# Kernel tuning notes

Hardware: AMD Instinct MI355X
Metric: run time of the kernel (lower is better)

## Reference

```python
import jax, jax.numpy as jnp
import numpy as np

B, H, W, CIN, CI = 2, 64, 64, 128, 128  # in_channels == inter_channels (required by final gating)
N = H * W
TEMP = 1.0
EPS = 1e-3  # tfa InstanceNormalization default epsilon


def _conv1x1(x, w, b):
    # x: (B,H,W,Cin), w: (Cin,Cout)
    return jnp.einsum('bhwc,cd->bhwd', x, w) + b


def _conv3x3_reflect(x, w, b):
    x = jnp.pad(x, ((0, 0), (1, 1), (1, 1), (0, 0)), mode='reflect')
    y = jax.lax.conv_general_dilated(x, w, (1, 1), 'VALID',
                                     dimension_numbers=('NHWC', 'HWIO', 'NHWC'))
    return y + b


def _instance_norm(x, gamma, beta):
    m = x.mean(axis=(1, 2), keepdims=True)
    v = x.var(axis=(1, 2), keepdims=True)
    return (x - m) * jax.lax.rsqrt(v + EPS) * gamma + beta


def setup_inputs() -> dict:
    key = jax.random.key(0)
    ks = jax.random.split(key, 16)
    p = lambda i, shape: 0.02 * jax.random.normal(ks[i], shape, jnp.float32)
    x = jax.random.normal(ks[0], (B, H, W, CIN), jnp.float32)
    mask = (jax.random.uniform(ks[1], (B, H, W, 1)) > 0.5).astype(jnp.float32)  # binary hole mask
    return dict(
        x=x, mask=mask,
        wg=p(2, (CIN, CI)), bg=jnp.zeros((CI,), jnp.float32),
        wt=p(3, (CIN, CI)), bt=jnp.zeros((CI,), jnp.float32),
        wp=p(4, (CIN, CI)), bp=jnp.zeros((CI,), jnp.float32),
        ww=p(5, (CI, CIN)), bw=jnp.zeros((CIN,), jnp.float32),
        res_w1=p(6, (3, 3, 3, CIN, CIN)), res_b1=jnp.zeros((3, CIN), jnp.float32),
        res_g1=jnp.ones((3, CIN), jnp.float32), res_be1=jnp.zeros((3, CIN), jnp.float32),
        res_w2=p(7, (3, 3, 3, CIN, CIN)), res_b2=jnp.zeros((3, CIN), jnp.float32),
        res_g2=jnp.ones((3, CIN), jnp.float32), res_be2=jnp.zeros((3, CIN), jnp.float32),
    )


def reference(x, mask, wg, bg, wt, bt, wp, bp, ww, bw,
              res_w1, res_b1, res_g1, res_be1,
              res_w2, res_b2, res_g2, res_be2):
    # projections, flatten spatial -> tokens
    g_x = _conv1x1(x, wg, bg).reshape(B, N, CI)      # (B,N,Ci)
    theta = _conv1x1(x, wt, bt).reshape(B, N, CI)    # (B,N,Ci)
    phi = _conv1x1(x, wp, bp).reshape(B, N, CI)      # (B,N,Ci)

    # f_div_C = softmax(theta . phi^T / T) over keys  -> (B,N,N), memory-dominant
    f_div_C = jax.nn.softmax(jnp.einsum('bnc,bmc->bnm', theta, phi) / TEMP, axis=2)

    # mask processing (bilinear resize to x's spatial size; identity here)
    inverted = 1.0 - mask
    m = jax.image.resize(mask, (B, H, W, 1), 'bilinear')
    m = jnp.where(m > 0.0, jnp.zeros_like(m), m)  # zero out any positively-masked pixel
    m = 1.0 - m                                   # 1 where strictly unmasked
    inverted = jax.image.resize(inverted, (B, H, W, 1), 'bilinear')
    m = m * inverted                              # (B,H,W,1)

    # gate attention columns by mask (broadcast over query rows == tf.repeat)
    f_div_C = m.reshape(B, 1, N) * f_div_C

    y = jnp.einsum('bnm,bmc->bnc', f_div_C, g_x).reshape(B, H, W, CI)
    w_y = _conv1x1(y, ww, bw)                     # (B,H,W,Cin)

    # 3 ResNet blocks: reflect-pad conv3x3 -> IN -> ReLU -> reflect-pad conv3x3 -> IN, + residual
    for i in range(3):
        h = jax.nn.relu(_instance_norm(_conv3x3_reflect(w_y, res_w1[i], res_b1[i]),
                                       res_g1[i], res_be1[i]))
        h = _instance_norm(_conv3x3_reflect(h, res_w2[i], res_b2[i]),
                           res_g2[i], res_be2[i])
        w_y = w_y + h

    # mode == 'combine': mask-gated blend of input and attention output
    z = m * x + (1.0 - m) * w_y
    return z
```

## Files before the change

### kernel.cpp

```cpp
#include <hip/hip_runtime.h>
#include <math.h>

constexpr int NB = 2;
constexpr int IMG = 64;
constexpr int CH = 128;
constexpr int NT = IMG * IMG;
constexpr int ATT_KSPLIT = 8;
constexpr int KPS = NT / ATT_KSPLIT;

typedef __bf16 bf16x8 __attribute__((ext_vector_type(8)));
typedef float f32x4 __attribute__((ext_vector_type(4)));

__device__ __forceinline__ unsigned f2bf(float x) {
  unsigned u = __float_as_uint(x);
  return (u + 0x7fffu + ((u >> 16) & 1u)) >> 16;
}
__device__ __forceinline__ float bf2f(unsigned h) {
  return __uint_as_float(h << 16);
}
__device__ __forceinline__ float maskval(float mk) {
  float mm = mk > 0.f ? 0.f : mk;
  return (1.f - mm) * (1.f - mk);
}

__global__ __launch_bounds__(256) void k_prepw(
    const float* __restrict__ rw1, const float* __restrict__ rw2,
    const float* __restrict__ wt_, const float* __restrict__ wp_,
    const float* __restrict__ wg_, const float* __restrict__ ww_,
    unsigned short* __restrict__ wfrag) {
  __shared__ float Ws[128][132];
  const int t = threadIdx.x, bx = blockIdx.x;
  const float* src;
  if (bx < 54) {
    int i2 = bx / 9, tap = bx - i2 * 9;
    int blk = i2 >> 1;
    src = ((i2 & 1) ? rw2 : rw1) + ((size_t)blk * 9 + tap) * 16384;
  } else {
    src = bx == 54 ? wt_ : bx == 55 ? wp_ : bx == 56 ? wg_ : ww_;
  }
#pragma unroll
  for (int k = 0; k < 16; ++k) {
    int i4 = t + 256 * k;
    int row = i4 >> 5, c4 = (i4 & 31) << 2;
    *(float4*)&Ws[row][c4] = *(const float4*)(src + (size_t)row * 128 + c4);
  }
  __syncthreads();
  unsigned short* dst = wfrag + (size_t)bx * 16384;
#pragma unroll
  for (int i = 0; i < 8; ++i) {
    int idx = t + 256 * i;
    int lane = idx & 63, k = (idx >> 6) & 3, cotile = idx >> 8;
    int lg = lane >> 4, lc = lane & 15;
    int co = cotile * 16 + lc, ci0 = k * 32 + lg * 8;
    unsigned u0 = f2bf(Ws[ci0 + 0][co]) | (f2bf(Ws[ci0 + 1][co]) << 16);
    unsigned u1 = f2bf(Ws[ci0 + 2][co]) | (f2bf(Ws[ci0 + 3][co]) << 16);
    unsigned u2 = f2bf(Ws[ci0 + 4][co]) | (f2bf(Ws[ci0 + 5][co]) << 16);
    unsigned u3 = f2bf(Ws[ci0 + 6][co]) | (f2bf(Ws[ci0 + 7][co]) << 16);
    *(uint4*)(dst + (size_t)idx * 8) = make_uint4(u0, u1, u2, u3);
  }
}

__global__ __launch_bounds__(256) void k_proj3(
    const float* __restrict__ x, const float* __restrict__ mask,
    const unsigned short* __restrict__ wf, const float* __restrict__ bt_,
    const float* __restrict__ bp_, const float* __restrict__ bg_,
    unsigned short* __restrict__ thb, unsigned short* __restrict__ phb,
    unsigned short* __restrict__ vtb) {
  __shared__ __align__(16) unsigned short Al[64 * 136];
  __shared__ __align__(16) unsigned short Tl[64 * 136];
  const int t = threadIdx.x, r0 = blockIdx.x * 64, b = r0 >> 12;

#pragma unroll
  for (int k = 0; k < 4; ++k) {
    int it = t + 256 * k;
    int row = it >> 4, g = it & 15;
    const float* s = x + (size_t)(r0 + row) * 128 + g * 8;
    float4 v0 = *(const float4*)s, v1 = *(const float4*)(s + 4);
    uint4 pk;
    pk.x = f2bf(v0.x) | (f2bf(v0.y) << 16);
    pk.y = f2bf(v0.z) | (f2bf(v0.w) << 16);
    pk.z = f2bf(v1.x) | (f2bf(v1.y) << 16);
    pk.w = f2bf(v1.z) | (f2bf(v1.w) << 16);
    *(uint4*)&Al[row * 136 + g * 8] = pk;
  }
  __syncthreads();

  const int w = t >> 6, lane = t & 63, lg = lane >> 4, lc = lane & 15;
  const int mw = w & 1, nw = w >> 1;
#pragma unroll
  for (int mat = 0; mat < 3; ++mat) {
    f32x4 acc[2][4];
#pragma unroll
    for (int m = 0; m < 2; ++m)
#pragma unroll
      for (int n = 0; n < 4; ++n)
#pragma unroll
        for (int r = 0; r < 4; ++r) acc[m][n][r] = 0.f;
    const unsigned short* wb =
        wf + (size_t)(54 + mat) * 16384 + (size_t)(nw * 4) * 2048 + lane * 8;
#pragma unroll
    for (int k = 0; k < 4; ++k) {
      bf16x8 a0 = *(const bf16x8*)&Al[(mw * 32 + lc) * 136 + k * 32 + lg * 8];
      bf16x8 a1 = *(const bf16x8*)&Al[(mw * 32 + 16 + lc) * 136 + k * 32 + lg * 8];
#pragma unroll
      for (int n = 0; n < 4; ++n) {
        bf16x8 bfr = *(const bf16x8*)(wb + n * 2048 + k * 512);
        acc[0][n] = __builtin_amdgcn_mfma_f32_16x16x32_bf16(a0, bfr, acc[0][n], 0, 0, 0);
        acc[1][n] = __builtin_amdgcn_mfma_f32_16x16x32_bf16(a1, bfr, acc[1][n], 0, 0, 0);
      }
    }
    const float* bs = mat == 0 ? bt_ : mat == 1 ? bp_ : bg_;
    float bbv[4];
#pragma unroll
    for (int n = 0; n < 4; ++n) bbv[n] = bs[nw * 64 + n * 16 + lc];

    if (mat < 2) {
      unsigned short* ob = mat == 0 ? thb : phb;
#pragma unroll
      for (int n = 0; n < 4; ++n) {
        int col = nw * 64 + n * 16 + lc;
#pragma unroll
        for (int m = 0; m < 2; ++m)
#pragma unroll
          for (int r = 0; r < 4; ++r) {
            int row = r0 + mw * 32 + m * 16 + lg * 4 + r;
            ob[(size_t)row * 128 + col] = (unsigned short)f2bf(acc[m][n][r] + bbv[n]);
          }
      }
    } else {
#pragma unroll
      for (int m = 0; m < 2; ++m)
#pragma unroll
        for (int r = 0; r < 4; ++r) {
          int rl = mw * 32 + m * 16 + lg * 4 + r;
          float mvv = maskval(mask[r0 + rl]);
#pragma unroll
          for (int n = 0; n < 4; ++n) {
            int col = nw * 64 + n * 16 + lc;
            Tl[rl * 136 + col] = (unsigned short)f2bf((acc[m][n][r] + bbv[n]) * mvv);
          }
        }
      __syncthreads();
      const int c = t >> 1, h = t & 1;
      unsigned buf[16];
#pragma unroll
      for (int j = 0; j < 16; ++j)
        buf[j] = (unsigned)Tl[(h * 32 + 2 * j) * 136 + c] |
                 ((unsigned)Tl[(h * 32 + 2 * j + 1) * 136 + c] << 16);
      const int key0 = r0 & (NT - 1);
      unsigned short* dst = vtb + ((size_t)b * CH + c) * NT + key0 + h * 32;
      uint4* d4 = (uint4*)dst;
#pragma unroll
      for (int q = 0; q < 4; ++q)
        d4[q] = make_uint4(buf[4 * q], buf[4 * q + 1], buf[4 * q + 2], buf[4 * q + 3]);
    }
  }
}

__global__ __launch_bounds__(256, 2) void k_attn(
    const unsigned short* __restrict__ theta, const unsigned short* __restrict__ phi,
    const unsigned short* __restrict__ vt, unsigned short* __restrict__ partO,
    float* __restrict__ partL) {
  __shared__ __align__(16) unsigned short Klds[64][136];
  __shared__ __align__(16) unsigned short Vtlds[128][72];
  __shared__ __align__(16) unsigned short Plds[4][32][72];

  const int t = threadIdx.x;
  const int bx = blockIdx.x;
  const int ks = bx & 7;
  const int qt = (bx >> 3) & 31;
  const int b = bx >> 8;
  const int w = t >> 6;
  const int lane = t & 63;
  const int lg = lane >> 4;
  const int lc = lane & 15;
  const int q0 = qt * 128 + w * 32;

  const unsigned short* thB = theta + (size_t)b * NT * CH;
  const unsigned short* phB = phi + (size_t)b * NT * CH;
  const unsigned short* vtB = vt + (size_t)b * CH * NT;

  bf16x8 qf[2][4];
#pragma unroll
  for (int q2 = 0; q2 < 2; ++q2)
#pragma unroll
    for (int k = 0; k < 4; ++k)
      qf[q2][k] = *(const bf16x8*)(thB + (size_t)(q0 + q2 * 16 + lc) * CH + k * 32 + lg * 8);

  f32x4 oacc[2][8];
#pragma unroll
  for (int q2 = 0; q2 < 2; ++q2)
#pragma unroll
    for (int c = 0; c < 8; ++c)
#pragma unroll
      for (int r = 0; r < 4; ++r) oacc[q2][c][r] = 0.f;
  float lsum[2][4] = {{0.f, 0.f, 0.f, 0.f}, {0.f, 0.f, 0.f, 0.f}};

  for (int kt = 0; kt < KPS; kt += 64) {
    const int key0 = ks * KPS + kt;
    __syncthreads();
#pragma unroll
    for (int i = 0; i < 4; ++i) {
      int idx = t + 256 * i;
      int row = idx >> 4, c8 = (idx & 15) * 8;
      *(uint4*)&Klds[row][c8] = *(const uint4*)(phB + (size_t)(key0 + row) * CH + c8);
      int rowv = idx >> 3, k8 = (idx & 7) * 8;
      *(uint4*)&Vtlds[rowv][k8] = *(const uint4*)(vtB + (size_t)rowv * NT + key0 + k8);
    }
    __syncthreads();

#pragma unroll
    for (int col = 0; col < 4; ++col) {
      bf16x8 kf[4];
#pragma unroll
      for (int k = 0; k < 4; ++k)
        kf[k] = *(const bf16x8*)&Klds[col * 16 + lc][k * 32 + lg * 8];
      f32x4 s0, s1;
#pragma unroll
      for (int r = 0; r < 4; ++r) { s0[r] = 0.f; s1[r] = 0.f; }
#pragma unroll
      for (int k = 0; k < 4; ++k) {
        s0 = __builtin_amdgcn_mfma_f32_16x16x32_bf16(qf[0][k], kf[k], s0, 0, 0, 0);
        s1 = __builtin_amdgcn_mfma_f32_16x16x32_bf16(qf[1][k], kf[k], s1, 0, 0, 0);
      }
#pragma unroll
      for (int r = 0; r < 4; ++r) {
        float p0 = __expf(s0[r]);
        lsum[0][r] += p0;
        Plds[w][lg * 4 + r][col * 16 + lc] = (unsigned short)f2bf(p0);
        float p1 = __expf(s1[r]);
        lsum[1][r] += p1;
        Plds[w][16 + lg * 4 + r][col * 16 + lc] = (unsigned short)f2bf(p1);
      }
    }

#pragma unroll
    for (int kp = 0; kp < 2; ++kp) {
      bf16x8 pa0 = *(const bf16x8*)&Plds[w][lc][kp * 32 + lg * 8];
      bf16x8 pa1 = *(const bf16x8*)&Plds[w][16 + lc][kp * 32 + lg * 8];
#pragma unroll
      for (int col = 0; col < 8; ++col) {
        bf16x8 vf = *(const bf16x8*)&Vtlds[col * 16 + lc][kp * 32 + lg * 8];
        oacc[0][col] = __builtin_amdgcn_mfma_f32_16x16x32_bf16(pa0, vf, oacc[0][col], 0, 0, 0);
        oacc[1][col] = __builtin_amdgcn_mfma_f32_16x16x32_bf16(pa1, vf, oacc[1][col], 0, 0, 0);
      }
    }
  }

#pragma unroll
  for (int off = 1; off < 16; off <<= 1)
#pragma unroll
    for (int q2 = 0; q2 < 2; ++q2)
#pragma unroll
      for (int r = 0; r < 4; ++r) lsum[q2][r] += __shfl_xor(lsum[q2][r], off);

  const size_t obase = ((size_t)ks * NB + b) * NT;
#pragma unroll
  for (int q2 = 0; q2 < 2; ++q2) {
#pragma unroll
    for (int col = 0; col < 8; ++col)
#pragma unroll
      for (int r = 0; r < 4; ++r) {
        int row = q0 + q2 * 16 + lg * 4 + r;
        partO[(obase + row) * CH + col * 16 + lc] = (unsigned short)f2bf(oacc[q2][col][r]);
      }
    if (lc == 0) {
#pragma unroll
      for (int r = 0; r < 4; ++r)
        partL[obase + q0 + q2 * 16 + lg * 4 + r] = lsum[q2][r];
    }
  }
}

__global__ __launch_bounds__(256) void k_gemmW(
    const unsigned short* __restrict__ partO, const float* __restrict__ partL,
    const unsigned short* __restrict__ wf, const float* __restrict__ bias,
    float* __restrict__ wy, unsigned short* __restrict__ wyb) {
  __shared__ __align__(16) unsigned short Al[64 * 136];
  __shared__ float linv[64];
  const int t = threadIdx.x, r0 = blockIdx.x * 64;

  if (t < 64) {
    float l = 0.f;
#pragma unroll
    for (int ks = 0; ks < ATT_KSPLIT; ++ks) l += partL[(size_t)ks * 8192 + r0 + t];
    linv[t] = 1.f / l;
  }
  __syncthreads();

#pragma unroll
  for (int i = 0; i < 4; ++i) {
    int it = t + 256 * i;
    int row = it >> 4, g = it & 15;
    float a[8] = {0.f, 0.f, 0.f, 0.f, 0.f, 0.f, 0.f, 0.f};
#pragma unroll
    for (int ks = 0; ks < ATT_KSPLIT; ++ks) {
      uint4 u = *(const uint4*)(partO + ((size_t)ks * 8192 + r0 + row) * 128 + g * 8);
      const unsigned* uw = (const unsigned*)&u;
#pragma unroll
      for (int q = 0; q < 4; ++q) {
        a[2 * q] += bf2f(uw[q] & 0xffffu);
        a[2 * q + 1] += bf2f(uw[q] >> 16);
      }
    }
    float s = linv[row];
    uint4 pk;
    pk.x = f2bf(a[0] * s) | (f2bf(a[1] * s) << 16);
    pk.y = f2bf(a[2] * s) | (f2bf(a[3] * s) << 16);
    pk.z = f2bf(a[4] * s) | (f2bf(a[5] * s) << 16);
    pk.w = f2bf(a[6] * s) | (f2bf(a[7] * s) << 16);
    *(uint4*)&Al[row * 136 + g * 8] = pk;
  }
  __syncthreads();

  const int w = t >> 6, lane = t & 63, lg = lane >> 4, lc = lane & 15;
  const int mw = w & 1, nw = w >> 1;
  f32x4 acc[2][4];
#pragma unroll
  for (int m = 0; m < 2; ++m)
#pragma unroll
    for (int n = 0; n < 4; ++n)
#pragma unroll
      for (int r = 0; r < 4; ++r) acc[m][n][r] = 0.f;
  const unsigned short* wb =
      wf + (size_t)57 * 16384 + (size_t)(nw * 4) * 2048 + lane * 8;
#pragma unroll
  for (int k = 0; k < 4; ++k) {
    bf16x8 a0 = *(const bf16x8*)&Al[(mw * 32 + lc) * 136 + k * 32 + lg * 8];
    bf16x8 a1 = *(const bf16x8*)&Al[(mw * 32 + 16 + lc) * 136 + k * 32 + lg * 8];
#pragma unroll
    for (int n = 0; n < 4; ++n) {
      bf16x8 bfr = *(const bf16x8*)(wb + n * 2048 + k * 512);
      acc[0][n] = __builtin_amdgcn_mfma_f32_16x16x32_bf16(a0, bfr, acc[0][n], 0, 0, 0);
      acc[1][n] = __builtin_amdgcn_mfma_f32_16x16x32_bf16(a1, bfr, acc[1][n], 0, 0, 0);
    }
  }
#pragma unroll
  for (int n = 0; n < 4; ++n) {
    int col = nw * 64 + n * 16 + lc;
    float bb = bias[col];
#pragma unroll
    for (int m = 0; m < 2; ++m)
#pragma unroll
      for (int r = 0; r < 4; ++r) {
        int row = r0 + mw * 32 + m * 16 + lg * 4 + r;
        float v = acc[m][n][r] + bb;
        wy[(size_t)row * 128 + col] = v;
        wyb[(size_t)row * 128 + col] = (unsigned short)f2bf(v);
      }
  }
}

template <bool AFFINE>
__global__ __launch_bounds__(512, 2) void k_conv(
    const unsigned short* __restrict__ act, const unsigned short* __restrict__ wf,
    const float* __restrict__ bias, const float* __restrict__ part_in,
    const float* __restrict__ gamma, const float* __restrict__ beta,
    unsigned short* __restrict__ outc, float* __restrict__ part_out) {
  __shared__ unsigned short Alds[3][34 * 136];
  __shared__ float red[256];
  __shared__ float Aff[2][128];

  const int t = threadIdx.x, bx = blockIdx.x;
  const int xh = bx & 1, y = (bx >> 1) & 63, b = bx >> 7;
  const int w = t >> 6, lane = t & 63, lg = lane >> 4, lc = lane & 15;
  const int x0 = xh * 32;
  const int coT = w;

  if constexpr (AFFINE) {
    if (t < 256) {
      const float4* p = (const float4*)(part_in + ((size_t)b * 256 + t) * 128);
      float s0 = 0.f, s1 = 0.f, s2 = 0.f, s3 = 0.f;
#pragma unroll 8
      for (int k = 0; k < 32; ++k) {
        float4 v = p[k];
        s0 += v.x; s1 += v.y; s2 += v.z; s3 += v.w;
      }
      red[t] = (s0 + s1) + (s2 + s3);
    }
    __syncthreads();
    if (t < 128) {
      float mean = red[2 * t] * (1.f / 4096.f);
      float var = red[2 * t + 1] * (1.f / 4096.f) - mean * mean;
      float a = gamma[t] * rsqrtf(var + 1e-3f);
      Aff[0][t] = a;
      Aff[1][t] = beta[t] - mean * a;
    }
    __syncthreads();
  }

  const unsigned short* actB = act + (size_t)b * NT * CH;
#pragma unroll
  for (int i = 0; i < 4; ++i) {
    int it = t + 512 * i;
    if (it < 1632) {
      int r = it / 544, rem = it - r * 544;
      int px = rem >> 4, g = rem & 15;
      int sy = y - 1 + r;
      sy = sy < 0 ? 1 : (sy > 63 ? 62 : sy);
      int sx = x0 - 1 + px;
      sx = sx < 0 ? 1 : (sx > 63 ? 62 : sx);
      uint4 v = *(const uint4*)(actB + (size_t)(sy * 64 + sx) * CH + g * 8);
      if constexpr (AFFINE) {
        int c0 = g * 8;
        unsigned* vw = (unsigned*)&v;
#pragma unroll
        for (int q = 0; q < 4; ++q) {
          float v0 = bf2f(vw[q] & 0xffffu), v1 = bf2f(vw[q] >> 16);
          v0 = fmaxf(0.f, fmaf(Aff[0][c0 + 2 * q], v0, Aff[1][c0 + 2 * q]));
          v1 = fmaxf(0.f, fmaf(Aff[0][c0 + 2 * q + 1], v1, Aff[1][c0 + 2 * q + 1]));
          vw[q] = f2bf(v0) | (f2bf(v1) << 16);
        }
      }
      *(uint4*)&Alds[r][px * 136 + g * 8] = v;
    }
  }
  __syncthreads();

  f32x4 acc[2];
#pragma unroll
  for (int m = 0; m < 2; ++m)
#pragma unroll
    for (int r = 0; r < 4; ++r) acc[m][r] = 0.f;

  const unsigned short* wbase = wf + (size_t)coT * 2048 + lane * 8;
  bf16x8 wc[4], wn[4];
#pragma unroll
  for (int k = 0; k < 4; ++k) wc[k] = *(const bf16x8*)(wbase + k * 512);
#pragma unroll
  for (int tap = 0; tap < 9; ++tap) {
    const int dy = tap / 3, dx = tap - dy * 3;
    if (tap < 8) {
#pragma unroll
      for (int k = 0; k < 4; ++k)
        wn[k] = *(const bf16x8*)(wbase + (size_t)(tap + 1) * 16384 + k * 512);
    }
#pragma unroll
    for (int k = 0; k < 4; ++k) {
      bf16x8 a0 = *(const bf16x8*)&Alds[dy][(dx + lc) * 136 + k * 32 + lg * 8];
      bf16x8 a1 = *(const bf16x8*)&Alds[dy][(dx + 16 + lc) * 136 + k * 32 + lg * 8];
      acc[0] = __builtin_amdgcn_mfma_f32_16x16x32_bf16(a0, wc[k], acc[0], 0, 0, 0);
      acc[1] = __builtin_amdgcn_mfma_f32_16x16x32_bf16(a1, wc[k], acc[1], 0, 0, 0);
    }
#pragma unroll
    for (int k = 0; k < 4; ++k) wc[k] = wn[k];
  }

  const int col = coT * 16 + lc;
  const float bs = bias[col];
  float sum = 0.f, sq = 0.f;
  unsigned short* outB = outc + (size_t)(b * NT + y * 64 + x0) * CH;
#pragma unroll
  for (int m = 0; m < 2; ++m)
#pragma unroll
    for (int r = 0; r < 4; ++r) {
      float v = acc[m][r] + bs;
      int px = m * 16 + lg * 4 + r;
      outB[(size_t)px * CH + col] = (unsigned short)f2bf(v);
      sum += v;
      sq = fmaf(v, v, sq);
    }
  sum += __shfl_xor(sum, 16);
  sum += __shfl_xor(sum, 32);
  sq += __shfl_xor(sq, 16);
  sq += __shfl_xor(sq, 32);
  if (lg == 0) {
    const int pg = y * 2 + xh;
    part_out[((size_t)(b * 128 + col) * 2 + 0) * 128 + pg] = sum;
    part_out[((size_t)(b * 128 + col) * 2 + 1) * 128 + pg] = sq;
  }
}

template <bool FINAL>
__global__ __launch_bounds__(256) void k_residual(
    const unsigned short* __restrict__ c2v, const float* __restrict__ part_in,
    const float* __restrict__ gamma, const float* __restrict__ beta,
    float* __restrict__ wy, unsigned short* __restrict__ wyb,
    const float* __restrict__ x, const float* __restrict__ mask,
    float* __restrict__ out) {
  __shared__ float red[256];
  __shared__ float AffA[128];
  __shared__ float AffB[128];
  const int t = threadIdx.x, bx = blockIdx.x;
  const int b = bx >> 8;

  {
    const float4* p = (const float4*)(part_in + ((size_t)b * 256 + t) * 128);
    float s0 = 0.f, s1 = 0.f, s2 = 0.f, s3 = 0.f;
#pragma unroll 8
    for (int k = 0; k < 32; ++k) {
      float4 v = p[k];
      s0 += v.x; s1 += v.y; s2 += v.z; s3 += v.w;
    }
    red[t] = (s0 + s1) + (s2 + s3);
  }
  __syncthreads();
  if (t < 128) {
    float mean = red[2 * t] * (1.f / 4096.f);
    float var = red[2 * t + 1] * (1.f / 4096.f) - mean * mean;
    float a = gamma[t] * rsqrtf(var + 1e-3f);
    AffA[t] = a;
    AffB[t] = beta[t] - mean * a;
  }
  __syncthreads();

  const int idx = bx * 256 + t;
  const int g = idx & 15;
  const int pixel = idx >> 4;
  const int c0 = g * 8;
  uint4 v = *(const uint4*)(c2v + (size_t)pixel * CH + c0);
  float* wp_ = wy + (size_t)pixel * CH + c0;
  float4 w0 = *(float4*)wp_, w1 = *(float4*)(wp_ + 4);
  float wv[8] = {w0.x, w0.y, w0.z, w0.w, w1.x, w1.y, w1.z, w1.w};
  const unsigned* vw = (const unsigned*)&v;
  float o[8];
#pragma unroll
  for (int q = 0; q < 8; ++q) {
    float cv = bf2f((q & 1) ? (vw[q >> 1] >> 16) : (vw[q >> 1] & 0xffffu));
    o[q] = wv[q] + fmaf(AffA[c0 + q], cv, AffB[c0 + q]);
  }
  if constexpr (FINAL) {
    const float m = maskval(mask[pixel]);
    const float* xp = x + (size_t)pixel * CH + c0;
    float4 x0 = *(const float4*)xp, x1 = *(const float4*)(xp + 4);
    float xv[8] = {x0.x, x0.y, x0.z, x0.w, x1.x, x1.y, x1.z, x1.w};
    float* op = out + (size_t)pixel * CH + c0;
    float r[8];
#pragma unroll
    for (int q = 0; q < 8; ++q) r[q] = m * xv[q] + (1.f - m) * o[q];
    *(float4*)op = make_float4(r[0], r[1], r[2], r[3]);
    *(float4*)(op + 4) = make_float4(r[4], r[5], r[6], r[7]);
  } else {
    *(float4*)wp_ = make_float4(o[0], o[1], o[2], o[3]);
    *(float4*)(wp_ + 4) = make_float4(o[4], o[5], o[6], o[7]);
    uint4 pk;
    pk.x = f2bf(o[0]) | (f2bf(o[1]) << 16);
    pk.y = f2bf(o[2]) | (f2bf(o[3]) << 16);
    pk.z = f2bf(o[4]) | (f2bf(o[5]) << 16);
    pk.w = f2bf(o[6]) | (f2bf(o[7]) << 16);
    *(uint4*)(wyb + (size_t)pixel * CH + c0) = pk;
  }
}

extern "C" void kernel_launch(void* const* d_in, const int* in_sizes, int n_in,
                              void* d_out, int out_size, void* d_ws, size_t ws_size,
                              hipStream_t stream) {
  (void)in_sizes; (void)n_in; (void)out_size; (void)ws_size;
  const float* x    = (const float*)d_in[0];
  const float* mask = (const float*)d_in[1];
  const float* wg   = (const float*)d_in[2];
  const float* bg   = (const float*)d_in[3];
  const float* wt   = (const float*)d_in[4];
  const float* bt   = (const float*)d_in[5];
  const float* wp   = (const float*)d_in[6];
  const float* bp   = (const float*)d_in[7];
  const float* ww   = (const float*)d_in[8];
  const float* bw   = (const float*)d_in[9];
  const float* rw1  = (const float*)d_in[10];
  const float* rb1  = (const float*)d_in[11];
  const float* rg1  = (const float*)d_in[12];
  const float* rbe1 = (const float*)d_in[13];
  const float* rw2  = (const float*)d_in[14];
  const float* rb2  = (const float*)d_in[15];
  const float* rg2  = (const float*)d_in[16];
  const float* rbe2 = (const float*)d_in[17];
  float* out = (float*)d_out;

  char* W = (char*)d_ws;
  unsigned short* wfrag = (unsigned short*)W;
  char* base = W + 2097152;
  unsigned short* thb   = (unsigned short*)(base);
  unsigned short* phb   = (unsigned short*)(base + 2097152);
  unsigned short* vtb   = (unsigned short*)(base + 2 * 2097152);
  float*          partL = (float*)(base + 3 * 2097152);
  unsigned short* partO = (unsigned short*)(base + 3 * 2097152 + 262144);
  float*          wy    = (float*)(base);
  unsigned short* wyb   = (unsigned short*)(base + 2 * 2097152);
  unsigned short* c1    = partO;
  unsigned short* c2    = (unsigned short*)((char*)partO + 2097152);
  float*          partA = (float*)((char*)partO + 2 * 2097152);
  float*          partB = (float*)((char*)partO + 2 * 2097152 + 262144);

  k_prepw<<<58, 256, 0, stream>>>(rw1, rw2, wt, wp, wg, ww, wfrag);
  k_proj3<<<128, 256, 0, stream>>>(x, mask, wfrag, bt, bp, bg, thb, phb, vtb);
  k_attn<<<512, 256, 0, stream>>>(thb, phb, vtb, partO, partL);
  k_gemmW<<<128, 256, 0, stream>>>(partO, partL, wfrag, bw, wy, wyb);

  for (int i = 0; i < 3; ++i) {
    const unsigned short* wf1 = wfrag + (size_t)(2 * i) * 9 * 16384;
    const unsigned short* wf2 = wfrag + (size_t)(2 * i + 1) * 9 * 16384;
    k_conv<false><<<256, 512, 0, stream>>>(wyb, wf1, rb1 + i * 128, nullptr,
                                           nullptr, nullptr, c1, partA);
    k_conv<true><<<256, 512, 0, stream>>>(c1, wf2, rb2 + i * 128, partA,
                                          rg1 + i * 128, rbe1 + i * 128, c2, partB);
    if (i < 2) {
      k_residual<false><<<512, 256, 0, stream>>>(c2, partB, rg2 + i * 128,
                                                 rbe2 + i * 128, wy, wyb,
                                                 nullptr, nullptr, nullptr);
    } else {
      k_residual<true><<<512, 256, 0, stream>>>(c2, partB, rg2 + i * 128,
                                                rbe2 + i * 128, wy, nullptr,
                                                x, mask, out);
    }
  }
}
```

Before: 153.1 us.

## Fuse residual conv chain into one persistent kernel with grid barriers

Replaces the nine separate conv and residual launches for the three ResNet blocks with a single persistent kernel of 256 blocks. The phases are separated by a software grid barrier built on an atomic counter, and the residual phase is remapped from 512 blocks of 256 threads to 256 blocks of 512. The aim is to remove per-launch overhead and the gaps between dependent kernels. In exchange it relies on all 256 blocks being co-resident to avoid deadlock, and adds atomic spin-wait and fence costs.

```diff
diff --git a/kernel.cpp b/kernel.cpp
--- a/kernel.cpp
+++ b/kernel.cpp
@@ -351,16 +351,25 @@
   }
 }
 
+__device__ __forceinline__ void gbar(unsigned* cnt, unsigned target) {
+  __syncthreads();
+  if (threadIdx.x == 0) {
+    __threadfence();
+    atomicAdd(cnt, 1u);
+    while (__hip_atomic_load(cnt, __ATOMIC_RELAXED, __HIP_MEMORY_SCOPE_AGENT) < target)
+      __builtin_amdgcn_s_sleep(2);
+  }
+  __syncthreads();
+  __threadfence();
+}
+
 template <bool AFFINE>
-__global__ __launch_bounds__(512, 2) void k_conv(
+__device__ __forceinline__ void conv_phase(
+    unsigned short* Alds, float* red, float* Aff,
     const unsigned short* __restrict__ act, const unsigned short* __restrict__ wf,
     const float* __restrict__ bias, const float* __restrict__ part_in,
     const float* __restrict__ gamma, const float* __restrict__ beta,
     unsigned short* __restrict__ outc, float* __restrict__ part_out) {
-  __shared__ unsigned short Alds[3][34 * 136];
-  __shared__ float red[256];
-  __shared__ float Aff[2][128];
-
   const int t = threadIdx.x, bx = blockIdx.x;
   const int xh = bx & 1, y = (bx >> 1) & 63, b = bx >> 7;
   const int w = t >> 6, lane = t & 63, lg = lane >> 4, lc = lane & 15;
@@ -383,8 +392,8 @@
       float mean = red[2 * t] * (1.f / 4096.f);
       float var = red[2 * t + 1] * (1.f / 4096.f) - mean * mean;
       float a = gamma[t] * rsqrtf(var + 1e-3f);
-      Aff[0][t] = a;
-      Aff[1][t] = beta[t] - mean * a;
+      Aff[t] = a;
+      Aff[128 + t] = beta[t] - mean * a;
     }
     __syncthreads();
   }
@@ -407,12 +416,12 @@
 #pragma unroll
         for (int q = 0; q < 4; ++q) {
           float v0 = bf2f(vw[q] & 0xffffu), v1 = bf2f(vw[q] >> 16);
-          v0 = fmaxf(0.f, fmaf(Aff[0][c0 + 2 * q], v0, Aff[1][c0 + 2 * q]));
-          v1 = fmaxf(0.f, fmaf(Aff[0][c0 + 2 * q + 1], v1, Aff[1][c0 + 2 * q + 1]));
+          v0 = fmaxf(0.f, fmaf(Aff[c0 + 2 * q], v0, Aff[128 + c0 + 2 * q]));
+          v1 = fmaxf(0.f, fmaf(Aff[c0 + 2 * q + 1], v1, Aff[128 + c0 + 2 * q + 1]));
           vw[q] = f2bf(v0) | (f2bf(v1) << 16);
         }
       }
-      *(uint4*)&Alds[r][px * 136 + g * 8] = v;
+      *(uint4*)&Alds[r * (34 * 136) + px * 136 + g * 8] = v;
     }
   }
   __syncthreads();
@@ -437,8 +446,8 @@
     }
 #pragma unroll
     for (int k = 0; k < 4; ++k) {
-      bf16x8 a0 = *(const bf16x8*)&Alds[dy][(dx + lc) * 136 + k * 32 + lg * 8];
-      bf16x8 a1 = *(const bf16x8*)&Alds[dy][(dx + 16 + lc) * 136 + k * 32 + lg * 8];
+      bf16x8 a0 = *(const bf16x8*)&Alds[dy * (34 * 136) + (dx + lc) * 136 + k * 32 + lg * 8];
+      bf16x8 a1 = *(const bf16x8*)&Alds[dy * (34 * 136) + (dx + 16 + lc) * 136 + k * 32 + lg * 8];
       acc[0] = __builtin_amdgcn_mfma_f32_16x16x32_bf16(a0, wc[k], acc[0], 0, 0, 0);
       acc[1] = __builtin_amdgcn_mfma_f32_16x16x32_bf16(a1, wc[k], acc[1], 0, 0, 0);
     }
@@ -471,20 +480,17 @@
   }
 }
 
-template <bool FINAL>
-__global__ __launch_bounds__(256) void k_residual(
+__device__ __forceinline__ void residual_phase(
+    bool final_, float* red, float* Aff,
     const unsigned short* __restrict__ c2v, const float* __restrict__ part_in,
     const float* __restrict__ gamma, const float* __restrict__ beta,
     float* __restrict__ wy, unsigned short* __restrict__ wyb,
     const float* __restrict__ x, const float* __restrict__ mask,
     float* __restrict__ out) {
-  __shared__ float red[256];
-  __shared__ float AffA[128];
-  __shared__ float AffB[128];
   const int t = threadIdx.x, bx = blockIdx.x;
-  const int b = bx >> 8;
-
-  {
+  const int b = bx >> 7;
+
+  if (t < 256) {
     const float4* p = (const float4*)(part_in + ((size_t)b * 256 + t) * 128);
     float s0 = 0.f, s1 = 0.f, s2 = 0.f, s3 = 0.f;
 #pragma unroll 8
@@ -499,12 +505,12 @@
     float mean = red[2 * t] * (1.f / 4096.f);
     float var = red[2 * t + 1] * (1.f / 4096.f) - mean * mean;
     float a = gamma[t] * rsqrtf(var + 1e-3f);
-    AffA[t] = a;
-    AffB[t] = beta[t] - mean * a;
-  }
-  __syncthreads();
-
-  const int idx = bx * 256 + t;
+    Aff[t] = a;
+    Aff[128 + t] = beta[t] - mean * a;
+  }
+  __syncthreads();
+
+  const int idx = bx * 512 + t;
   const int g = idx & 15;
   const int pixel = idx >> 4;
   const int c0 = g * 8;
@@ -517,9 +523,9 @@
 #pragma unroll
   for (int q = 0; q < 8; ++q) {
     float cv = bf2f((q & 1) ? (vw[q >> 1] >> 16) : (vw[q >> 1] & 0xffffu));
-    o[q] = wv[q] + fmaf(AffA[c0 + q], cv, AffB[c0 + q]);
-  }
-  if constexpr (FINAL) {
+    o[q] = wv[q] + fmaf(Aff[c0 + q], cv, Aff[128 + c0 + q]);
+  }
+  if (final_) {
     const float m = maskval(mask[pixel]);
     const float* xp = x + (size_t)pixel * CH + c0;
     float4 x0 = *(const float4*)xp, x1 = *(const float4*)(xp + 4);
@@ -539,6 +545,36 @@
     pk.z = f2bf(o[4]) | (f2bf(o[5]) << 16);
     pk.w = f2bf(o[6]) | (f2bf(o[7]) << 16);
     *(uint4*)(wyb + (size_t)pixel * CH + c0) = pk;
+  }
+}
+
+__global__ __launch_bounds__(512) void k_reschain(
+    const unsigned short* __restrict__ wfrag,
+    const float* __restrict__ rb1, const float* __restrict__ rb2,
+    const float* __restrict__ rg1, const float* __restrict__ rbe1,
+    const float* __restrict__ rg2, const float* __restrict__ rbe2,
+    unsigned short* __restrict__ wyb, unsigned short* __restrict__ c1,
+    unsigned short* __restrict__ c2, float* __restrict__ partA,
+    float* __restrict__ partB, float* __restrict__ wy,
+    const float* __restrict__ x, const float* __restrict__ mask,
+    float* __restrict__ out, unsigned* __restrict__ cnt) {
+  __shared__ __align__(16) unsigned short Alds[3 * 34 * 136];
+  __shared__ float red[256];
+  __shared__ float Aff[2 * 128];
+
+  unsigned target = 0;
+  for (int i = 0; i < 3; ++i) {
+    const unsigned short* wf1 = wfrag + (size_t)(2 * i) * 9 * 16384;
+    const unsigned short* wf2 = wfrag + (size_t)(2 * i + 1) * 9 * 16384;
+    conv_phase<false>(Alds, red, Aff, wyb, wf1, rb1 + i * 128, nullptr, nullptr,
+                      nullptr, c1, partA);
+    target += 256; gbar(cnt, target);
+    conv_phase<true>(Alds, red, Aff, c1, wf2, rb2 + i * 128, partA,
+                     rg1 + i * 128, rbe1 + i * 128, c2, partB);
+    target += 256; gbar(cnt, target);
+    residual_phase(i == 2, red, Aff, c2, partB, rg2 + i * 128, rbe2 + i * 128,
+                   wy, wyb, x, mask, out);
+    if (i < 2) { target += 256; gbar(cnt, target); }
   }
 }
 
@@ -574,6 +610,7 @@
   unsigned short* vtb   = (unsigned short*)(base + 2 * 2097152);
   float*          partL = (float*)(base + 3 * 2097152);
   unsigned short* partO = (unsigned short*)(base + 3 * 2097152 + 262144);
+  unsigned*       cnt   = (unsigned*)(base + 3 * 2097152 + 262144 + 16777216);
   float*          wy    = (float*)(base);
   unsigned short* wyb   = (unsigned short*)(base + 2 * 2097152);
   unsigned short* c1    = partO;
@@ -581,26 +618,12 @@
   float*          partA = (float*)((char*)partO + 2 * 2097152);
   float*          partB = (float*)((char*)partO + 2 * 2097152 + 262144);
 
+  hipMemsetAsync(cnt, 0, 64, stream);
   k_prepw<<<58, 256, 0, stream>>>(rw1, rw2, wt, wp, wg, ww, wfrag);
   k_proj3<<<128, 256, 0, stream>>>(x, mask, wfrag, bt, bp, bg, thb, phb, vtb);
   k_attn<<<512, 256, 0, stream>>>(thb, phb, vtb, partO, partL);
   k_gemmW<<<128, 256, 0, stream>>>(partO, partL, wfrag, bw, wy, wyb);
-
-  for (int i = 0; i < 3; ++i) {
-    const unsigned short* wf1 = wfrag + (size_t)(2 * i) * 9 * 16384;
-    const unsigned short* wf2 = wfrag + (size_t)(2 * i + 1) * 9 * 16384;
-    k_conv<false><<<256, 512, 0, stream>>>(wyb, wf1, rb1 + i * 128, nullptr,
-                                           nullptr, nullptr, c1, partA);
-    k_conv<true><<<256, 512, 0, stream>>>(c1, wf2, rb2 + i * 128, partA,
-                                          rg1 + i * 128, rbe1 + i * 128, c2, partB);
-    if (i < 2) {
-      k_residual<false><<<512, 256, 0, stream>>>(c2, partB, rg2 + i * 128,
-                                                 rbe2 + i * 128, wy, wyb,
-                                                 nullptr, nullptr, nullptr);
-    } else {
-      k_residual<true><<<512, 256, 0, stream>>>(c2, partB, rg2 + i * 128,
-                                                rbe2 + i * 128, wy, nullptr,
-                                                x, mask, out);
-    }
-  }
-}
+  k_reschain<<<256, 512, 0, stream>>>(wfrag, rb1, rb2, rg1, rbe1, rg2, rbe2,
+                                      wyb, c1, c2, partA, partB, wy,
+                                      x, mask, out, cnt);
+}
```

After: 515.2 us. +236.6%, slower.

## Fuse residual update into next conv's input staging and split weight prep

Applied to the files above, without the earlier changes.

The intermediate residual kernels are removed. The next conv kernel in MODE 2 now reads wy and c2, applies the instance-norm affine, adds the residual, writes the updated fp32 wy (center row only) to a ping-pong buffer, and stages the bf16 result in LDS. This drops two launches and a bf16 write/read round trip, at the cost of redundant halo recomputation and extra fp32 loads inside the conv's staging. Weight prep is also split into four slices per tile (232 blocks instead of 58) for more parallelism.

```diff
diff --git a/kernel.cpp b/kernel.cpp
--- a/kernel.cpp
+++ b/kernel.cpp
@@ -28,34 +28,37 @@
     const float* __restrict__ wt_, const float* __restrict__ wp_,
     const float* __restrict__ wg_, const float* __restrict__ ww_,
     unsigned short* __restrict__ wfrag) {
-  __shared__ float Ws[128][132];
-  const int t = threadIdx.x, bx = blockIdx.x;
+  __shared__ float Ws[32][132];
+  const int t = threadIdx.x;
+  const int tile = blockIdx.x >> 2, slice = blockIdx.x & 3;
   const float* src;
-  if (bx < 54) {
-    int i2 = bx / 9, tap = bx - i2 * 9;
+  if (tile < 54) {
+    int i2 = tile / 9, tap = tile - i2 * 9;
     int blk = i2 >> 1;
     src = ((i2 & 1) ? rw2 : rw1) + ((size_t)blk * 9 + tap) * 16384;
   } else {
-    src = bx == 54 ? wt_ : bx == 55 ? wp_ : bx == 56 ? wg_ : ww_;
-  }
-#pragma unroll
-  for (int k = 0; k < 16; ++k) {
+    src = tile == 54 ? wt_ : tile == 55 ? wp_ : tile == 56 ? wg_ : ww_;
+  }
+#pragma unroll
+  for (int k = 0; k < 4; ++k) {
     int i4 = t + 256 * k;
     int row = i4 >> 5, c4 = (i4 & 31) << 2;
-    *(float4*)&Ws[row][c4] = *(const float4*)(src + (size_t)row * 128 + c4);
+    *(float4*)&Ws[row][c4] =
+        *(const float4*)(src + (size_t)(slice * 32 + row) * 128 + c4);
   }
   __syncthreads();
-  unsigned short* dst = wfrag + (size_t)bx * 16384;
-#pragma unroll
-  for (int i = 0; i < 8; ++i) {
-    int idx = t + 256 * i;
-    int lane = idx & 63, k = (idx >> 6) & 3, cotile = idx >> 8;
+  unsigned short* dst = wfrag + (size_t)tile * 16384;
+#pragma unroll
+  for (int i = 0; i < 2; ++i) {
+    int it = t + 256 * i;
+    int cotile = it >> 6, lane = it & 63;
     int lg = lane >> 4, lc = lane & 15;
-    int co = cotile * 16 + lc, ci0 = k * 32 + lg * 8;
-    unsigned u0 = f2bf(Ws[ci0 + 0][co]) | (f2bf(Ws[ci0 + 1][co]) << 16);
-    unsigned u1 = f2bf(Ws[ci0 + 2][co]) | (f2bf(Ws[ci0 + 3][co]) << 16);
-    unsigned u2 = f2bf(Ws[ci0 + 4][co]) | (f2bf(Ws[ci0 + 5][co]) << 16);
-    unsigned u3 = f2bf(Ws[ci0 + 6][co]) | (f2bf(Ws[ci0 + 7][co]) << 16);
+    int co = cotile * 16 + lc, r0 = lg * 8;
+    unsigned u0 = f2bf(Ws[r0 + 0][co]) | (f2bf(Ws[r0 + 1][co]) << 16);
+    unsigned u1 = f2bf(Ws[r0 + 2][co]) | (f2bf(Ws[r0 + 3][co]) << 16);
+    unsigned u2 = f2bf(Ws[r0 + 4][co]) | (f2bf(Ws[r0 + 5][co]) << 16);
+    unsigned u3 = f2bf(Ws[r0 + 6][co]) | (f2bf(Ws[r0 + 7][co]) << 16);
+    int idx = cotile * 256 + slice * 64 + lane;
     *(uint4*)(dst + (size_t)idx * 8) = make_uint4(u0, u1, u2, u3);
   }
 }
@@ -351,12 +354,13 @@
   }
 }
 
-template <bool AFFINE>
+template <int MODE>
 __global__ __launch_bounds__(512, 2) void k_conv(
     const unsigned short* __restrict__ act, const unsigned short* __restrict__ wf,
     const float* __restrict__ bias, const float* __restrict__ part_in,
     const float* __restrict__ gamma, const float* __restrict__ beta,
-    unsigned short* __restrict__ outc, float* __restrict__ part_out) {
+    unsigned short* __restrict__ outc, float* __restrict__ part_out,
+    const float* __restrict__ wy_in, float* __restrict__ wy_out) {
   __shared__ unsigned short Alds[3][34 * 136];
   __shared__ float red[256];
   __shared__ float Aff[2][128];
@@ -367,7 +371,7 @@
   const int x0 = xh * 32;
   const int coT = w;
 
-  if constexpr (AFFINE) {
+  if constexpr (MODE >= 1) {
     if (t < 256) {
       const float4* p = (const float4*)(part_in + ((size_t)b * 256 + t) * 128);
       float s0 = 0.f, s1 = 0.f, s2 = 0.f, s3 = 0.f;
@@ -400,8 +404,9 @@
       sy = sy < 0 ? 1 : (sy > 63 ? 62 : sy);
       int sx = x0 - 1 + px;
       sx = sx < 0 ? 1 : (sx > 63 ? 62 : sx);
-      uint4 v = *(const uint4*)(actB + (size_t)(sy * 64 + sx) * CH + g * 8);
-      if constexpr (AFFINE) {
+      const int lpix = sy * 64 + sx;
+      uint4 v = *(const uint4*)(actB + (size_t)lpix * CH + g * 8);
+      if constexpr (MODE == 1) {
         int c0 = g * 8;
         unsigned* vw = (unsigned*)&v;
 #pragma unroll
@@ -411,6 +416,30 @@
           v1 = fmaxf(0.f, fmaf(Aff[0][c0 + 2 * q + 1], v1, Aff[1][c0 + 2 * q + 1]));
           vw[q] = f2bf(v0) | (f2bf(v1) << 16);
         }
+      } else if constexpr (MODE == 2) {
+        int c0 = g * 8;
+        const size_t gpix = (size_t)b * NT + lpix;
+        const float* wpin = wy_in + gpix * CH + c0;
+        float4 w0 = *(const float4*)wpin, w1 = *(const float4*)(wpin + 4);
+        float wv[8] = {w0.x, w0.y, w0.z, w0.w, w1.x, w1.y, w1.z, w1.w};
+        const unsigned* vw = (const unsigned*)&v;
+        float o[8];
+#pragma unroll
+        for (int q = 0; q < 8; ++q) {
+          float cv = bf2f((q & 1) ? (vw[q >> 1] >> 16) : (vw[q >> 1] & 0xffffu));
+          o[q] = wv[q] + fmaf(Aff[0][c0 + q], cv, Aff[1][c0 + q]);
+        }
+        if (r == 1 && px >= 1 && px < 33) {
+          float* wpo = wy_out + gpix * CH + c0;
+          *(float4*)wpo = make_float4(o[0], o[1], o[2], o[3]);
+          *(float4*)(wpo + 4) = make_float4(o[4], o[5], o[6], o[7]);
+        }
+        uint4 pk;
+        pk.x = f2bf(o[0]) | (f2bf(o[1]) << 16);
+        pk.y = f2bf(o[2]) | (f2bf(o[3]) << 16);
+        pk.z = f2bf(o[4]) | (f2bf(o[5]) << 16);
+        pk.w = f2bf(o[6]) | (f2bf(o[7]) << 16);
+        v = pk;
       }
       *(uint4*)&Alds[r][px * 136 + g * 8] = v;
     }
@@ -471,13 +500,11 @@
   }
 }
 
-template <bool FINAL>
-__global__ __launch_bounds__(256) void k_residual(
+__global__ __launch_bounds__(256) void k_residual_final(
     const unsigned short* __restrict__ c2v, const float* __restrict__ part_in,
     const float* __restrict__ gamma, const float* __restrict__ beta,
-    float* __restrict__ wy, unsigned short* __restrict__ wyb,
-    const float* __restrict__ x, const float* __restrict__ mask,
-    float* __restrict__ out) {
+    const float* __restrict__ wy, const float* __restrict__ x,
+    const float* __restrict__ mask, float* __restrict__ out) {
   __shared__ float red[256];
   __shared__ float AffA[128];
   __shared__ float AffB[128];
@@ -509,8 +536,8 @@
   const int pixel = idx >> 4;
   const int c0 = g * 8;
   uint4 v = *(const uint4*)(c2v + (size_t)pixel * CH + c0);
-  float* wp_ = wy + (size_t)pixel * CH + c0;
-  float4 w0 = *(float4*)wp_, w1 = *(float4*)(wp_ + 4);
+  const float* wp_ = wy + (size_t)pixel * CH + c0;
+  float4 w0 = *(const float4*)wp_, w1 = *(const float4*)(wp_ + 4);
   float wv[8] = {w0.x, w0.y, w0.z, w0.w, w1.x, w1.y, w1.z, w1.w};
   const unsigned* vw = (const unsigned*)&v;
   float o[8];
@@ -519,27 +546,16 @@
     float cv = bf2f((q & 1) ? (vw[q >> 1] >> 16) : (vw[q >> 1] & 0xffffu));
     o[q] = wv[q] + fmaf(AffA[c0 + q], cv, AffB[c0 + q]);
   }
-  if constexpr (FINAL) {
-    const float m = maskval(mask[pixel]);
-    const float* xp = x + (size_t)pixel * CH + c0;
-    float4 x0 = *(const float4*)xp, x1 = *(const float4*)(xp + 4);
-    float xv[8] = {x0.x, x0.y, x0.z, x0.w, x1.x, x1.y, x1.z, x1.w};
-    float* op = out + (size_t)pixel * CH + c0;
-    float r[8];
-#pragma unroll
-    for (int q = 0; q < 8; ++q) r[q] = m * xv[q] + (1.f - m) * o[q];
-    *(float4*)op = make_float4(r[0], r[1], r[2], r[3]);
-    *(float4*)(op + 4) = make_float4(r[4], r[5], r[6], r[7]);
-  } else {
-    *(float4*)wp_ = make_float4(o[0], o[1], o[2], o[3]);
-    *(float4*)(wp_ + 4) = make_float4(o[4], o[5], o[6], o[7]);
-    uint4 pk;
-    pk.x = f2bf(o[0]) | (f2bf(o[1]) << 16);
-    pk.y = f2bf(o[2]) | (f2bf(o[3]) << 16);
-    pk.z = f2bf(o[4]) | (f2bf(o[5]) << 16);
-    pk.w = f2bf(o[6]) | (f2bf(o[7]) << 16);
-    *(uint4*)(wyb + (size_t)pixel * CH + c0) = pk;
-  }
+  const float m = maskval(mask[pixel]);
+  const float* xp = x + (size_t)pixel * CH + c0;
+  float4 x0 = *(const float4*)xp, x1 = *(const float4*)(xp + 4);
+  float xv[8] = {x0.x, x0.y, x0.z, x0.w, x1.x, x1.y, x1.z, x1.w};
+  float* op = out + (size_t)pixel * CH + c0;
+  float r[8];
+#pragma unroll
+  for (int q = 0; q < 8; ++q) r[q] = m * xv[q] + (1.f - m) * o[q];
+  *(float4*)op = make_float4(r[0], r[1], r[2], r[3]);
+  *(float4*)(op + 4) = make_float4(r[4], r[5], r[6], r[7]);
 }
 
 extern "C" void kernel_launch(void* const* d_in, const int* in_sizes, int n_in,
@@ -574,33 +590,38 @@
   unsigned short* vtb   = (unsigned short*)(base + 2 * 2097152);
   float*          partL = (float*)(base + 3 * 2097152);
   unsigned short* partO = (unsigned short*)(base + 3 * 2097152 + 262144);
-  float*          wy    = (float*)(base);
+  float*          wy0   = (float*)(base);
   unsigned short* wyb   = (unsigned short*)(base + 2 * 2097152);
   unsigned short* c1    = partO;
   unsigned short* c2    = (unsigned short*)((char*)partO + 2097152);
   float*          partA = (float*)((char*)partO + 2 * 2097152);
   float*          partB = (float*)((char*)partO + 2 * 2097152 + 262144);
-
-  k_prepw<<<58, 256, 0, stream>>>(rw1, rw2, wt, wp, wg, ww, wfrag);
+  float*          wy1   = (float*)((char*)partO + 5 * 1048576);
+
+  k_prepw<<<232, 256, 0, stream>>>(rw1, rw2, wt, wp, wg, ww, wfrag);
   k_proj3<<<128, 256, 0, stream>>>(x, mask, wfrag, bt, bp, bg, thb, phb, vtb);
   k_attn<<<512, 256, 0, stream>>>(thb, phb, vtb, partO, partL);
-  k_gemmW<<<128, 256, 0, stream>>>(partO, partL, wfrag, bw, wy, wyb);
-
-  for (int i = 0; i < 3; ++i) {
-    const unsigned short* wf1 = wfrag + (size_t)(2 * i) * 9 * 16384;
-    const unsigned short* wf2 = wfrag + (size_t)(2 * i + 1) * 9 * 16384;
-    k_conv<false><<<256, 512, 0, stream>>>(wyb, wf1, rb1 + i * 128, nullptr,
-                                           nullptr, nullptr, c1, partA);
-    k_conv<true><<<256, 512, 0, stream>>>(c1, wf2, rb2 + i * 128, partA,
-                                          rg1 + i * 128, rbe1 + i * 128, c2, partB);
-    if (i < 2) {
-      k_residual<false><<<512, 256, 0, stream>>>(c2, partB, rg2 + i * 128,
-                                                 rbe2 + i * 128, wy, wyb,
-                                                 nullptr, nullptr, nullptr);
-    } else {
-      k_residual<true><<<512, 256, 0, stream>>>(c2, partB, rg2 + i * 128,
-                                                rbe2 + i * 128, wy, nullptr,
-                                                x, mask, out);
-    }
-  }
-}
+  k_gemmW<<<128, 256, 0, stream>>>(partO, partL, wfrag, bw, wy0, wyb);
+
+  const unsigned short* wf1_0 = wfrag;
+  const unsigned short* wf2_0 = wfrag + (size_t)1 * 9 * 16384;
+  const unsigned short* wf1_1 = wfrag + (size_t)2 * 9 * 16384;
+  const unsigned short* wf2_1 = wfrag + (size_t)3 * 9 * 16384;
+  const unsigned short* wf1_2 = wfrag + (size_t)4 * 9 * 16384;
+  const unsigned short* wf2_2 = wfrag + (size_t)5 * 9 * 16384;
+
+  k_conv<0><<<256, 512, 0, stream>>>(wyb, wf1_0, rb1, nullptr, nullptr, nullptr,
+                                     c1, partA, nullptr, nullptr);
+  k_conv<1><<<256, 512, 0, stream>>>(c1, wf2_0, rb2, partA, rg1, rbe1,
+                                     c2, partB, nullptr, nullptr);
+  k_conv<2><<<256, 512, 0, stream>>>(c2, wf1_1, rb1 + 128, partB, rg2, rbe2,
+                                     c1, partA, wy0, wy1);
+  k_conv<1><<<256, 512, 0, stream>>>(c1, wf2_1, rb2 + 128, partA, rg1 + 128,
+                                     rbe1 + 128, c2, partB, nullptr, nullptr);
+  k_conv<2><<<256, 512, 0, stream>>>(c2, wf1_2, rb1 + 256, partB, rg2 + 128,
+                                     rbe2 + 128, c1, partA, wy1, wy0);
+  k_conv<1><<<256, 512, 0, stream>>>(c1, wf2_2, rb2 + 256, partA, rg1 + 256,
+                                     rbe1 + 256, c2, partB, nullptr, nullptr);
+  k_residual_final<<<512, 256, 0, stream>>>(c2, partB, rg2 + 256, rbe2 + 256,
+                                            wy0, x, mask, out);
+}
```

Result: faster. 139.7 us (-8.8%).
